# Kernel tuning notes

Measured on AMD Instinct MI355X. Metric: run time of the kernel, lower is better.

## Reference

```python
import jax, jax.numpy as jnp
import numpy as np

CLASSES = 21
IOU_THRESH = 0.5
ALPHA = 0.25   # focal loss alpha
GAMMA = 2.0    # focal loss gamma
SL1_BETA = 1.0 # torch SmoothL1Loss default beta
CLS_W = 1.0
REG_W = 1.0
NUM_ANCHORS = 98304
NUM_TARGETS = 1024


def _compute_iou(boxes_a, boxes_b):
    # boxes_a: [T,4], boxes_b: [A,4] in (x1,y1,x2,y2) -> [T,A]
    lt = jnp.maximum(boxes_a[:, None, :2], boxes_b[None, :, :2])
    rb = jnp.minimum(boxes_a[:, None, 2:], boxes_b[None, :, 2:])
    wh = jnp.clip(rb - lt, 0.0)
    inter = wh[..., 0] * wh[..., 1]
    area_a = (boxes_a[:, 2] - boxes_a[:, 0]) * (boxes_a[:, 3] - boxes_a[:, 1])
    area_b = (boxes_b[:, 2] - boxes_b[:, 0]) * (boxes_b[:, 3] - boxes_b[:, 1])
    union = area_a[:, None] + area_b[None, :] - inter
    return inter / jnp.maximum(union, 1e-8)


def _encode(boxes, anchors):
    bw = boxes[:, 2] - boxes[:, 0]
    bh = boxes[:, 3] - boxes[:, 1]
    bcx = boxes[:, 0] + 0.5 * bw
    bcy = boxes[:, 1] + 0.5 * bh
    aw = anchors[:, 2] - anchors[:, 0]
    ah = anchors[:, 3] - anchors[:, 1]
    acx = anchors[:, 0] + 0.5 * aw
    acy = anchors[:, 1] + 0.5 * ah
    tx = (bcx - acx) / aw
    ty = (bcy - acy) / ah
    tw = jnp.log(jnp.maximum(bw, 1e-8) / aw)
    th = jnp.log(jnp.maximum(bh, 1e-8) / ah)
    return jnp.stack([tx, ty, tw, th], axis=1)


def _focal_loss(logits, targets):
    # elementwise sigmoid focal loss (no reduction)
    p = jax.nn.sigmoid(logits)
    # numerically stable BCE with logits
    ce = jnp.maximum(logits, 0.0) - logits * targets + jnp.log1p(jnp.exp(-jnp.abs(logits)))
    p_t = p * targets + (1.0 - p) * (1.0 - targets)
    alpha_t = ALPHA * targets + (1.0 - ALPHA) * (1.0 - targets)
    return alpha_t * (1.0 - p_t) ** GAMMA * ce


def _smooth_l1(diff):
    ad = jnp.abs(diff)
    return jnp.where(ad < SL1_BETA, 0.5 * diff * diff / SL1_BETA, ad - 0.5 * SL1_BETA)


def setup_inputs() -> dict:
    key = jax.random.key(0)
    kA, kW, kT, kJ, kL, kC, kB = jax.random.split(key, 7)
    A, T = NUM_ANCHORS, NUM_TARGETS
    centers = jax.random.uniform(kA, (A, 2), minval=0.15, maxval=0.85)
    sizes = jax.random.uniform(kW, (A, 2), minval=0.05, maxval=0.30)
    anchors = jnp.concatenate([centers - 0.5 * sizes, centers + 0.5 * sizes], axis=1)
    # targets = jittered anchors so IoU >= 0.5 matches exist
    idx = jax.random.randint(kT, (T,), 0, A)
    jitter = jax.random.uniform(kJ, (T, 4), minval=-0.01, maxval=0.01)
    target_boxes = anchors[idx] + jitter
    target_labels = jax.random.randint(kL, (T,), 0, CLASSES)
    classification_preds = jax.random.normal(kC, (A, CLASSES), dtype=jnp.float32)
    boxes_preds = jax.random.normal(kB, (A, 4), dtype=jnp.float32)
    return {
        'classification_preds': classification_preds,
        'boxes_preds': boxes_preds,
        'anchors': anchors,
        'target_boxes': target_boxes,
        'target_labels': target_labels,
    }


def reference(classification_preds, boxes_preds, anchors, target_boxes, target_labels):
    iou = _compute_iou(target_boxes, anchors)  # [T, A]

    # anchor-side matching -> classification targets
    max_iou_for_anchors = jnp.max(iou, axis=0)          # [A]
    target_ids_for_anchors = jnp.argmax(iou, axis=0)     # [A]
    positive_mask = max_iou_for_anchors >= IOU_THRESH    # [A] bool
    n_pos = jnp.sum(positive_mask.astype(jnp.float32))
    onehot = jax.nn.one_hot(target_labels[target_ids_for_anchors], CLASSES, dtype=jnp.float32)
    cls_targets = jnp.where(positive_mask[:, None], onehot, 0.0)
    cls_loss = jnp.sum(_focal_loss(classification_preds, cls_targets)) / n_pos

    max_iou_for_targets = jnp.max(iou, axis=1)          # [T]
    anchor_ids_for_targets = jnp.argmax(iou, axis=1)     # [T]
    t_mask = (max_iou_for_targets >= IOU_THRESH).astype(jnp.float32)  # [T]
    matched_anchors = anchors[anchor_ids_for_targets]    # [T,4]
    encoded = _encode(target_boxes, matched_anchors)     # [T,4]
    pred = boxes_preds[anchor_ids_for_targets]           # [T,4]
    diff = (pred - encoded) * t_mask[:, None]
    n_match = jnp.maximum(jnp.sum(t_mask), 1.0)
    reg_loss = jnp.sum(_smooth_l1(diff)) / (n_match * 4.0)  # mean over matched elements

    w_cls = cls_loss * CLS_W
    w_reg = reg_loss * REG_W
    return (w_cls + w_reg, w_cls, w_reg)
```

## Files before the change

### kernel.cpp

```cpp
#include <hip/hip_runtime.h>
#include <stdint.h>

#define NA 98304
#define NT 1024
#define NC 21
#define ACH 192
#define TCH 8
#define NBLK (ACH * TCH)
#define HI_MIN 0xBF000000u
#define POISON 0xAAAAAAAAu


__device__ __forceinline__ float f0(float x) {
    const float ax = fabsf(x);
    const float u  = __expf(-ax);
    const float ce = fmaxf(x, 0.f) + __logf(1.f + u);
    const float p  = (x >= 0.f ? 1.f : u) / (1.f + u);
    return 0.75f * p * p * ce;
}
__device__ __forceinline__ float f1(float x) {
    const float ax = fabsf(x);
    const float u  = __expf(-ax);
    const float ce = fmaxf(x, 0.f) - x + __logf(1.f + u);
    const float p  = (x >= 0.f ? 1.f : u) / (1.f + u);
    const float q  = 1.f - p;
    return 0.25f * q * q * ce;
}
__device__ __forceinline__ unsigned long long mk_key(float iou, unsigned int idx) {
    return ((unsigned long long)(__float_as_uint(iou) | 0x80000000u) << 32) |
           (unsigned long long)(0xFFFFFFFFu - idx);
}
__device__ __forceinline__ float smooth_l1(float d) {
    const float ad = fabsf(d);
    return (ad < 1.f) ? 0.5f * d * d : ad - 0.5f;
}
__device__ __forceinline__ unsigned long long aload64(const unsigned long long* p) {
    return __hip_atomic_load(p, __ATOMIC_RELAXED, __HIP_MEMORY_SCOPE_AGENT);
}
__device__ __forceinline__ float aloadf(const float* p) {
    return __hip_atomic_load(p, __ATOMIC_RELAXED, __HIP_MEMORY_SCOPE_AGENT);
}
__device__ __forceinline__ int aloadi(const int* p) {
    return __hip_atomic_load(p, __ATOMIC_RELAXED, __HIP_MEMORY_SCOPE_AGENT);
}

__global__ __launch_bounds__(256) void k_all(
    const float* __restrict__ preds,
    const float4* __restrict__ preds4,
    const int* __restrict__ tlabels,
    const float4* __restrict__ anchors,
    const float4* __restrict__ tboxes,
    const float4* __restrict__ bpreds,
    unsigned long long* __restrict__ akeys,
    unsigned long long* __restrict__ tkeys,
    float* __restrict__ f0_part,
    float* __restrict__ corr_part,
    int* __restrict__ npos_part,
    unsigned* __restrict__ done_ac,
    unsigned* __restrict__ done2,
    float* __restrict__ out)
{
    __shared__ float4 s_t[128];
    __shared__ unsigned long long s_tk[128];
    __shared__ float s_f[4];
    __shared__ int   s_last, s_fin;
    __shared__ float s_a[4];
    __shared__ int   s_c[4];
    __shared__ double s_d[4];
    __shared__ int    s_i[4];
    __shared__ float  s_s[4], s_m[4];

    const int tid   = threadIdx.x;
    const int ac    = blockIdx.x;
    const int L     = blockIdx.y * ACH + ac;
    const int tbase = blockIdx.y * 128;
    const int a0    = ac * 512 + tid;
    const int a1    = a0 + 256;
    const int lane  = tid & 63, wid = tid >> 6;

    if (tid < 128) {
        s_t[tid]  = tboxes[tbase + tid];
        s_tk[tid] = 0ull;
    }
    const float4 A0 = anchors[a0];
    const float4 A1 = anchors[a1];

    float facc;
    {
        const int pb = L * 336;
        const float4 v0 = preds4[pb + tid];
        facc = (f0(v0.x) + f0(v0.y)) + (f0(v0.z) + f0(v0.w));
        if (tid < 80) {
            const float4 v1 = preds4[pb + 256 + tid];
            facc += (f0(v1.x) + f0(v1.y)) + (f0(v1.z) + f0(v1.w));
        }
    }
    __syncthreads();

    const float ar0 = (A0.z - A0.x) * (A0.w - A0.y);
    const float ar1 = (A1.z - A1.x) * (A1.w - A1.y);

    float b0 = 0.f, b1 = 0.f;
    int   i0 = -1,  i1 = -1;

    #pragma unroll 4
    for (int t = 0; t < 128; ++t) {
        const float4 tb = s_t[t];
        const float sa = (tb.z - tb.x) * (tb.w - tb.y);
        {
            const float lx = fmaxf(A0.x, tb.x);
            const float ly = fmaxf(A0.y, tb.y);
            const float rx = fminf(A0.z, tb.z);
            const float ry = fminf(A0.w, tb.w);
            const float w  = fmaxf(rx - lx, 0.f);
            const float h  = fmaxf(ry - ly, 0.f);
            const float inter = w * h;
            const float uni = (ar0 + sa) - inter;
            if (__builtin_expect(inter + inter >= uni, 0)) {
                const float iou = inter / uni;
                if (iou > b0) { b0 = iou; i0 = t; }
                atomicMax(&s_tk[t], mk_key(iou, (unsigned int)a0));
            }
        }
        {
            const float lx = fmaxf(A1.x, tb.x);
            const float ly = fmaxf(A1.y, tb.y);
            const float rx = fminf(A1.z, tb.z);
            const float ry = fminf(A1.w, tb.w);
            const float w  = fmaxf(rx - lx, 0.f);
            const float h  = fmaxf(ry - ly, 0.f);
            const float inter = w * h;
            const float uni = (ar1 + sa) - inter;
            if (__builtin_expect(inter + inter >= uni, 0)) {
                const float iou = inter / uni;
                if (iou > b1) { b1 = iou; i1 = t; }
                atomicMax(&s_tk[t], mk_key(iou, (unsigned int)a1));
            }
        }
    }

    if (i0 >= 0) atomicMax(&akeys[a0], mk_key(b0, (unsigned int)(tbase + i0)));
    if (i1 >= 0) atomicMax(&akeys[a1], mk_key(b1, (unsigned int)(tbase + i1)));

    for (int o = 32; o > 0; o >>= 1) facc += __shfl_down(facc, o);
    if (lane == 0) s_f[wid] = facc;

    __syncthreads();
    if (tid < 128) {
        const unsigned long long tk = s_tk[tid];
        if (tk != 0ull) atomicMax(&tkeys[tbase + tid], tk);
    }
    if (tid == 0)
        __hip_atomic_store(&f0_part[L], s_f[0] + s_f[1] + s_f[2] + s_f[3],
                           __ATOMIC_RELAXED, __HIP_MEMORY_SCOPE_AGENT);

    __syncthreads();
    if (tid == 0) {
        __threadfence();
        s_last = (atomicAdd(&done_ac[ac], 1u) == POISON + TCH - 1);
    }
    __syncthreads();
    if (!s_last) return;
    __builtin_amdgcn_fence(__ATOMIC_ACQUIRE, "agent");

    float acc = 0.f;
    int   cnt = 0;
    {
        const unsigned long long k = aload64(&akeys[a0]);
        if ((unsigned int)(k >> 32) >= HI_MIN) {
            cnt = 1;
            const int lab = tlabels[0xFFFFFFFFu - (unsigned int)k];
            const float x = preds[a0 * NC + lab];
            acc += f1(x) - f0(x);
        }
    }
    {
        const unsigned long long k = aload64(&akeys[a1]);
        if ((unsigned int)(k >> 32) >= HI_MIN) {
            cnt += 1;
            const int lab = tlabels[0xFFFFFFFFu - (unsigned int)k];
            const float x = preds[a1 * NC + lab];
            acc += f1(x) - f0(x);
        }
    }
    if (tid < TCH) acc += aloadf(&f0_part[ac + tid * ACH]);

    for (int o = 32; o > 0; o >>= 1) {
        acc += __shfl_down(acc, o);
        cnt += __shfl_down(cnt, o);
    }
    if (lane == 0) { s_a[wid] = acc; s_c[wid] = cnt; }
    __syncthreads();
    if (tid == 0) {
        __hip_atomic_store(&corr_part[ac], s_a[0] + s_a[1] + s_a[2] + s_a[3],
                           __ATOMIC_RELAXED, __HIP_MEMORY_SCOPE_AGENT);
        __hip_atomic_store(&npos_part[ac], s_c[0] + s_c[1] + s_c[2] + s_c[3],
                           __ATOMIC_RELAXED, __HIP_MEMORY_SCOPE_AGENT);
        __threadfence();
        s_fin = (atomicAdd(done2, 1u) == POISON + ACH - 1);
    }
    __syncthreads();
    if (!s_fin) return;
    __builtin_amdgcn_fence(__ATOMIC_ACQUIRE, "agent");

    double cl = 0.0;
    int    np = 0;
    if (tid < ACH) {
        cl = (double)aloadf(&corr_part[tid]);
        np = aloadi(&npos_part[tid]);
    }
    float s = 0.f, m = 0.f;
    #pragma unroll
    for (int j = 0; j < 4; ++j) {
        const int t = tid + 256 * j;
        const unsigned long long key = aload64(&tkeys[t]);
        if ((unsigned int)(key >> 32) >= HI_MIN) {
            const unsigned int ga = 0xFFFFFFFFu - (unsigned int)key;
            const float4 tb  = tboxes[t];
            const float4 abx = anchors[ga];
            const float4 pb  = bpreds[ga];
            const float bw = tb.z - tb.x, bh = tb.w - tb.y;
            const float bcx = tb.x + 0.5f * bw, bcy = tb.y + 0.5f * bh;
            const float aw = abx.z - abx.x, ah = abx.w - abx.y;
            const float acx = abx.x + 0.5f * aw, acy = abx.y + 0.5f * ah;
            const float tx = (bcx - acx) / aw;
            const float ty = (bcy - acy) / ah;
            const float tw = logf(fmaxf(bw, 1e-8f) / aw);
            const float th = logf(fmaxf(bh, 1e-8f) / ah);
            s += smooth_l1(pb.x - tx) + smooth_l1(pb.y - ty) +
                 smooth_l1(pb.z - tw) + smooth_l1(pb.w - th);
            m += 1.f;
        }
    }
    for (int o = 32; o > 0; o >>= 1) {
        cl += __shfl_down(cl, o);
        np += __shfl_down(np, o);
        s  += __shfl_down(s, o);
        m  += __shfl_down(m, o);
    }
    __syncthreads();
    if (lane == 0) { s_d[wid] = cl; s_i[wid] = np; s_s[wid] = s; s_m[wid] = m; }
    __syncthreads();
    if (tid == 0) {
        const double cls_sum = s_d[0] + s_d[1] + s_d[2] + s_d[3];
        const int    npos    = s_i[0] + s_i[1] + s_i[2] + s_i[3];
        const float  rs      = s_s[0] + s_s[1] + s_s[2] + s_s[3];
        const float  rm      = s_m[0] + s_m[1] + s_m[2] + s_m[3];
        const float cls = (float)(cls_sum / (double)npos);
        const float reg = rs / (fmaxf(rm, 1.f) * 4.f);
        out[0] = cls + reg;
        out[1] = cls;
        out[2] = reg;
    }
}

extern "C" void kernel_launch(void* const* d_in, const int* in_sizes, int n_in,
                              void* d_out, int out_size, void* d_ws, size_t ws_size,
                              hipStream_t stream) {
    const float*  preds   = (const float*)d_in[0];
    const float4* preds4  = (const float4*)d_in[0];
    const float4* bpreds  = (const float4*)d_in[1];
    const float4* anchors = (const float4*)d_in[2];
    const float4* tboxes  = (const float4*)d_in[3];
    const int*    tlabels = (const int*)d_in[4];

    char* ws = (char*)d_ws;
    unsigned* done2     = (unsigned*)(ws + 0);
    unsigned* done_ac   = (unsigned*)(ws + 64);
    float*    f0_part   = (float*)(ws + 1024);
    float*    corr_part = (float*)(ws + 7168);
    int*      npos_part = (int*)(ws + 7936);
    unsigned long long* tkeys = (unsigned long long*)(ws + 12288);
    unsigned long long* akeys = (unsigned long long*)(ws + 24576);

    k_all<<<dim3(ACH, TCH), 256, 0, stream>>>(
        preds, preds4, tlabels, anchors, tboxes, bpreds,
        akeys, tkeys, f0_part, corr_part, npos_part,
        done_ac, done2, (float*)d_out);
}
```

Measured before the change: 140.5 us.

## Bucket-sort anchors and targets by x-center to prune IoU pair loop

Adds three pre-kernels that bucket anchors and targets by x-center (histogram, scan, scatter), so each block in the main kernel handles spatially coherent anchors. Each block then computes a wave-wide x-range and loops only over the sorted targets whose bucket overlaps it, skipping pairs that cannot reach IoU 0.5. Tie-breaking is rewritten to use original target indices so argmax semantics are kept. The cost is three extra launches, global atomics for the scatter, and indirect anchor loads. Pruning correctness depends on the bucket mapping and the fixed 2e-3 margin covering the box geometry, which is tied to the input center range of 0.15 to 0.85.

```diff
diff --git a/kernel.cpp b/kernel.cpp
--- a/kernel.cpp
+++ b/kernel.cpp
@@ -43,6 +43,78 @@
 __device__ __forceinline__ int aloadi(const int* p) {
     return __hip_atomic_load(p, __ATOMIC_RELAXED, __HIP_MEMORY_SCOPE_AGENT);
 }
+__device__ __forceinline__ int buck(float cx) {
+    const int b = (int)((cx - 0.15f) * (256.0f / 0.7f));
+    return min(max(b, 0), 255);
+}
+
+__global__ __launch_bounds__(256) void k_sort1(
+    const float4* __restrict__ anchors, const float4* __restrict__ tboxes,
+    unsigned* __restrict__ g_ahist, int* __restrict__ t_off,
+    float4* __restrict__ st_box, int* __restrict__ st_orig)
+{
+    const int tid = threadIdx.x;
+    if (blockIdx.x == 384) {
+        __shared__ int h[256], cur[256];
+        h[tid] = 0;
+        __syncthreads();
+        float4 tb[4]; int bb[4];
+        #pragma unroll
+        for (int j = 0; j < 4; ++j) {
+            tb[j] = tboxes[tid + j * 256];
+            bb[j] = buck(0.5f * (tb[j].x + tb[j].z));
+            atomicAdd(&h[bb[j]], 1);
+        }
+        __syncthreads();
+        if (tid == 0) {
+            int s = 0;
+            for (int i = 0; i < 256; ++i) { cur[i] = s; t_off[i] = s; s += h[i]; }
+            t_off[256] = s;
+        }
+        __syncthreads();
+        #pragma unroll
+        for (int j = 0; j < 4; ++j) {
+            const int pos = atomicAdd(&cur[bb[j]], 1);
+            st_box[pos]  = tb[j];
+            st_orig[pos] = tid + j * 256;
+        }
+    } else {
+        __shared__ int h[256];
+        h[tid] = 0;
+        __syncthreads();
+        const float4 ab = anchors[blockIdx.x * 256 + tid];
+        atomicAdd(&h[buck(0.5f * (ab.x + ab.z))], 1);
+        __syncthreads();
+        if (h[tid]) atomicAdd(&g_ahist[tid], (unsigned)h[tid]);
+    }
+}
+
+__global__ __launch_bounds__(256) void k_scan(
+    const unsigned* __restrict__ g_ahist, unsigned* __restrict__ g_acur)
+{
+    __shared__ unsigned v[256];
+    const int tid = threadIdx.x;
+    const unsigned cnt = g_ahist[tid] - POISON;
+    v[tid] = cnt;
+    __syncthreads();
+    for (int off = 1; off < 256; off <<= 1) {
+        const unsigned x = (tid >= off) ? v[tid - off] : 0u;
+        __syncthreads();
+        v[tid] += x;
+        __syncthreads();
+    }
+    g_acur[tid] = v[tid] - cnt;
+}
+
+__global__ __launch_bounds__(256) void k_scat(
+    const float4* __restrict__ anchors, unsigned* __restrict__ g_acur,
+    int* __restrict__ sa_orig)
+{
+    const int a = blockIdx.x * 256 + threadIdx.x;
+    const float4 ab = anchors[a];
+    const unsigned pos = atomicAdd(&g_acur[buck(0.5f * (ab.x + ab.z))], 1u);
+    sa_orig[pos] = a;
+}
 
 __global__ __launch_bounds__(256) void k_all(
     const float* __restrict__ preds,
@@ -51,6 +123,10 @@
     const float4* __restrict__ anchors,
     const float4* __restrict__ tboxes,
     const float4* __restrict__ bpreds,
+    const int* __restrict__ sa_orig,
+    const float4* __restrict__ st_box,
+    const int* __restrict__ st_orig,
+    const int* __restrict__ t_off,
     unsigned long long* __restrict__ akeys,
     unsigned long long* __restrict__ tkeys,
     float* __restrict__ f0_part,
@@ -61,6 +137,7 @@
     float* __restrict__ out)
 {
     __shared__ float4 s_t[128];
+    __shared__ int    s_to[128];
     __shared__ unsigned long long s_tk[128];
     __shared__ float s_f[4];
     __shared__ int   s_last, s_fin;
@@ -74,16 +151,17 @@
     const int ac    = blockIdx.x;
     const int L     = blockIdx.y * ACH + ac;
     const int tbase = blockIdx.y * 128;
-    const int a0    = ac * 512 + tid;
-    const int a1    = a0 + 256;
     const int lane  = tid & 63, wid = tid >> 6;
 
     if (tid < 128) {
-        s_t[tid]  = tboxes[tbase + tid];
+        s_t[tid]  = st_box[tbase + tid];
+        s_to[tid] = st_orig[tbase + tid];
         s_tk[tid] = 0ull;
     }
-    const float4 A0 = anchors[a0];
-    const float4 A1 = anchors[a1];
+    const unsigned oa0 = (unsigned)sa_orig[ac * 512 + tid];
+    const unsigned oa1 = (unsigned)sa_orig[ac * 512 + tid + 256];
+    const float4 A0 = anchors[oa0];
+    const float4 A1 = anchors[oa1];
 
     float facc;
     {
@@ -100,47 +178,54 @@
     const float ar0 = (A0.z - A0.x) * (A0.w - A0.y);
     const float ar1 = (A1.z - A1.x) * (A1.w - A1.y);
 
+    float wlo, whi;
+    {
+        wlo = fminf(A0.x, A1.x) - 2e-3f;
+        whi = fmaxf(A0.z, A1.z) + 2e-3f;
+        #pragma unroll
+        for (int o = 1; o < 64; o <<= 1) {
+            wlo = fminf(wlo, __shfl_xor(wlo, o));
+            whi = fmaxf(whi, __shfl_xor(whi, o));
+        }
+    }
+    const int ilo = max(t_off[buck(wlo)], tbase);
+    const int ihi = min(t_off[buck(whi) + 1], tbase + 128);
+
     float b0 = 0.f, b1 = 0.f;
-    int   i0 = -1,  i1 = -1;
+    unsigned o0 = 0xFFFFFFFFu, o1 = 0xFFFFFFFFu;
 
     #pragma unroll 4
-    for (int t = 0; t < 128; ++t) {
+    for (int t = ilo - tbase; t < ihi - tbase; ++t) {
         const float4 tb = s_t[t];
         const float sa = (tb.z - tb.x) * (tb.w - tb.y);
         {
-            const float lx = fmaxf(A0.x, tb.x);
-            const float ly = fmaxf(A0.y, tb.y);
-            const float rx = fminf(A0.z, tb.z);
-            const float ry = fminf(A0.w, tb.w);
-            const float w  = fmaxf(rx - lx, 0.f);
-            const float h  = fmaxf(ry - ly, 0.f);
+            const float w  = fmaxf(fminf(A0.z, tb.z) - fmaxf(A0.x, tb.x), 0.f);
+            const float h  = fmaxf(fminf(A0.w, tb.w) - fmaxf(A0.y, tb.y), 0.f);
             const float inter = w * h;
             const float uni = (ar0 + sa) - inter;
             if (__builtin_expect(inter + inter >= uni, 0)) {
                 const float iou = inter / uni;
-                if (iou > b0) { b0 = iou; i0 = t; }
-                atomicMax(&s_tk[t], mk_key(iou, (unsigned int)a0));
+                const unsigned to = (unsigned)s_to[t];
+                if (iou > b0 || (iou == b0 && to < o0)) { b0 = iou; o0 = to; }
+                atomicMax(&s_tk[t], mk_key(iou, oa0));
             }
         }
         {
-            const float lx = fmaxf(A1.x, tb.x);
-            const float ly = fmaxf(A1.y, tb.y);
-            const float rx = fminf(A1.z, tb.z);
-            const float ry = fminf(A1.w, tb.w);
-            const float w  = fmaxf(rx - lx, 0.f);
-            const float h  = fmaxf(ry - ly, 0.f);
+            const float w  = fmaxf(fminf(A1.z, tb.z) - fmaxf(A1.x, tb.x), 0.f);
+            const float h  = fmaxf(fminf(A1.w, tb.w) - fmaxf(A1.y, tb.y), 0.f);
             const float inter = w * h;
             const float uni = (ar1 + sa) - inter;
             if (__builtin_expect(inter + inter >= uni, 0)) {
                 const float iou = inter / uni;
-                if (iou > b1) { b1 = iou; i1 = t; }
-                atomicMax(&s_tk[t], mk_key(iou, (unsigned int)a1));
+                const unsigned to = (unsigned)s_to[t];
+                if (iou > b1 || (iou == b1 && to < o1)) { b1 = iou; o1 = to; }
+                atomicMax(&s_tk[t], mk_key(iou, oa1));
             }
         }
     }
 
-    if (i0 >= 0) atomicMax(&akeys[a0], mk_key(b0, (unsigned int)(tbase + i0)));
-    if (i1 >= 0) atomicMax(&akeys[a1], mk_key(b1, (unsigned int)(tbase + i1)));
+    if (o0 != 0xFFFFFFFFu) atomicMax(&akeys[oa0], mk_key(b0, o0));
+    if (o1 != 0xFFFFFFFFu) atomicMax(&akeys[oa1], mk_key(b1, o1));
 
     for (int o = 32; o > 0; o >>= 1) facc += __shfl_down(facc, o);
     if (lane == 0) s_f[wid] = facc;
@@ -148,7 +233,7 @@
     __syncthreads();
     if (tid < 128) {
         const unsigned long long tk = s_tk[tid];
-        if (tk != 0ull) atomicMax(&tkeys[tbase + tid], tk);
+        if (tk != 0ull) atomicMax(&tkeys[s_to[tid]], tk);
     }
     if (tid == 0)
         __hip_atomic_store(&f0_part[L], s_f[0] + s_f[1] + s_f[2] + s_f[3],
@@ -166,20 +251,20 @@
     float acc = 0.f;
     int   cnt = 0;
     {
-        const unsigned long long k = aload64(&akeys[a0]);
+        const unsigned long long k = aload64(&akeys[oa0]);
         if ((unsigned int)(k >> 32) >= HI_MIN) {
             cnt = 1;
             const int lab = tlabels[0xFFFFFFFFu - (unsigned int)k];
-            const float x = preds[a0 * NC + lab];
+            const float x = preds[oa0 * NC + lab];
             acc += f1(x) - f0(x);
         }
     }
     {
-        const unsigned long long k = aload64(&akeys[a1]);
+        const unsigned long long k = aload64(&akeys[oa1]);
         if ((unsigned int)(k >> 32) >= HI_MIN) {
             cnt += 1;
             const int lab = tlabels[0xFFFFFFFFu - (unsigned int)k];
-            const float x = preds[a1 * NC + lab];
+            const float x = preds[oa1 * NC + lab];
             acc += f1(x) - f0(x);
         }
     }
@@ -265,16 +350,27 @@
     const int*    tlabels = (const int*)d_in[4];
 
     char* ws = (char*)d_ws;
-    unsigned* done2     = (unsigned*)(ws + 0);
-    unsigned* done_ac   = (unsigned*)(ws + 64);
-    float*    f0_part   = (float*)(ws + 1024);
-    float*    corr_part = (float*)(ws + 7168);
-    int*      npos_part = (int*)(ws + 7936);
+    unsigned* g_ahist   = (unsigned*)(ws + 0);
+    unsigned* g_acur    = (unsigned*)(ws + 1024);
+    int*      t_off     = (int*)(ws + 2048);
+    unsigned* done2     = (unsigned*)(ws + 3584);
+    unsigned* done_ac   = (unsigned*)(ws + 3648);
+    float*    f0_part   = (float*)(ws + 4608);
+    float*    corr_part = (float*)(ws + 10752);
+    int*      npos_part = (int*)(ws + 11520);
     unsigned long long* tkeys = (unsigned long long*)(ws + 12288);
+    int*      st_orig   = (int*)(ws + 20480);
     unsigned long long* akeys = (unsigned long long*)(ws + 24576);
-
+    float4*   st_box    = (float4*)(ws + 811008);
+    int*      sa_orig   = (int*)(ws + 827392);
+
+    k_sort1<<<385, 256, 0, stream>>>(anchors, tboxes, g_ahist, t_off,
+                                     st_box, st_orig);
+    k_scan<<<1, 256, 0, stream>>>(g_ahist, g_acur);
+    k_scat<<<384, 256, 0, stream>>>(anchors, g_acur, sa_orig);
     k_all<<<dim3(ACH, TCH), 256, 0, stream>>>(
         preds, preds4, tlabels, anchors, tboxes, bpreds,
+        sa_orig, st_box, st_orig, t_off,
         akeys, tkeys, f0_part, corr_part, npos_part,
         done_ac, done2, (float*)d_out);
 }
```

Result: slower. 191.5 us (+36.3%).
